# Optimization experiments

Hardware: AMD Instinct MI355X
Metric: run time of the kernel (lower is better)

The kernel has to match this reference:

```python
import jax, jax.numpy as jnp
import numpy as np

N_NODES = 100000
N_EDGES = 1000000
D = 64            # in_channels == heads*hidden_channels
OUT = 64          # out_channels
L = 3             # local_layers
RVQ = 3           # residual VQ levels per layer
CODES = 16
BN_EPS = 1e-5
COMMIT_W = 0.25


def _l2n(v, eps=1e-12):
    return v / (jnp.linalg.norm(v, axis=-1, keepdims=True) + eps)


def setup_inputs() -> dict:
    key = jax.random.key(0)
    ks = jax.random.split(key, 16)
    s = 1.0 / np.sqrt(D)
    inp = {
        "x": jax.random.normal(ks[0], (N_NODES, D), jnp.float32),
        "edge_index": jax.random.randint(ks[1], (2, N_EDGES), 0, N_NODES, jnp.int64),
        # SAGEConv: lin_l (applied to mean-aggregated neighbors, with bias), lin_r (root, no bias)
        "Wa": jax.random.uniform(ks[2], (L, D, D), jnp.float32, -s, s),
        "ba": jax.random.uniform(ks[3], (L, D), jnp.float32, -s, s),
        "Wr": jax.random.uniform(ks[4], (L, D, D), jnp.float32, -s, s),
        # skip Linear per layer
        "Wl": jax.random.uniform(ks[5], (L, D, D), jnp.float32, -s, s),
        "bl": jax.random.uniform(ks[6], (L, D), jnp.float32, -s, s),
        # BatchNorm affine
        "gamma": jnp.ones((L, D), jnp.float32),
        "beta": jnp.zeros((L, D), jnp.float32),
        # residual-VQ codebooks: [layer, rvq_level, codes, dim]
        "codebooks": jax.random.normal(ks[7], (L, RVQ, CODES, D), jnp.float32),
        # heads
        "Wp": jax.random.uniform(ks[8], (D, OUT), jnp.float32, -s, s),
        "bp": jax.random.uniform(ks[9], (OUT,), jnp.float32, -s, s),
        "Wg": jax.random.uniform(ks[10], (D, L * RVQ), jnp.float32, -s, s),
        "bg": jax.random.uniform(ks[11], (L * RVQ,), jnp.float32, -s, s),
    }
    return inp


def _sage_conv(x, src, dst, Wa, ba, Wr):
    # mean aggregation of source features onto destinations
    summed = jax.ops.segment_sum(x[src], dst, num_segments=N_NODES)
    cnt = jax.ops.segment_sum(jnp.ones((src.shape[0],), x.dtype), dst, num_segments=N_NODES)
    mean = summed / jnp.maximum(cnt, 1.0)[:, None]
    out = mean @ Wa + ba + x @ Wr
    return _l2n(out)  # normalize=True


def _residual_vq(x, cbs):
    # cosine-sim residual VQ, 3 levels; returns (quantized_sum, ids [N,RVQ], commit_loss)
    residual = x
    quant = jnp.zeros_like(x)
    loss = jnp.zeros((), x.dtype)
    ids = []
    for r in range(RVQ):
        cb = _l2n(cbs[r])                       # [CODES, D]
        sim = _l2n(residual) @ cb.T             # [N, CODES]
        idx = jnp.argmax(sim, axis=-1)          # [N]
        q = cb[idx]                             # [N, D]
        loss = loss + COMMIT_W * jnp.mean((jax.lax.stop_gradient(q) - residual) ** 2)
        q_st = residual + jax.lax.stop_gradient(q - residual)  # straight-through
        quant = quant + q_st
        residual = residual - jax.lax.stop_gradient(q)
        ids.append(idx)
    return quant, jnp.stack(ids, axis=1), loss


def reference(x, edge_index, Wa, ba, Wr, Wl, bl, gamma, beta, codebooks, Wp, bp, Wg, bg):
    src, dst = edge_index[0], edge_index[1]
    h = x  # in_dropout: identity at inference
    x_local = jnp.zeros((N_NODES, D), x.dtype)
    total_commit = jnp.zeros((), x.dtype)
    id_list = []
    for i in range(L):
        h = _sage_conv(h, src, dst, Wa[i], ba[i], Wr[i]) + (h @ Wl[i] + bl[i])
        # BatchNorm1d (batch statistics)
        mu = jnp.mean(h, axis=0)
        var = jnp.var(h, axis=0)
        h = (h - mu) * jax.lax.rsqrt(var + BN_EPS) * gamma[i] + beta[i]
        h = jax.nn.relu(h)  # dropout: identity at inference
        x_local = x_local + h
        _, ids, closs = _residual_vq(h, codebooks[i])
        total_commit = total_commit + closs
        id_list.append(ids)
    id_concat = jnp.concatenate(id_list, axis=1)  # [N, L*RVQ]
    gnn_id = x_local @ Wg + bg
    pred = x_local @ Wp + bp
    return (pred, total_commit, id_concat, gnn_id)
```

## Files before the change

kernel.cpp:

```cpp
#include <hip/hip_runtime.h>
#include <math.h>

#define NN 100000
#define NE 1000000
#define D 64
#define L 3
#define RVQ 3
#define CODES 16
#define BN_EPS 1e-5f
#define COMMIT_W 0.25f

#define GRID_A 2048

#define OFS_ROWPTR 0
#define OFS_CNT    100016
#define OFS_CURSOR 200032
#define OFS_BSUMS  300048
#define OFS_BOFFS  300176
#define OFS_STATS  300304
#define OFS_CSR    300800
#define OFS_HA     1300800
#define OFS_HB     7700800
#define OFS_XLOC   14100800
#define OFS_PART   20500800

#define OUT_PRED   0
#define OUT_COMMIT (NN * D)
#define OUT_IDS    (NN * D + 1)
#define OUT_GNN    (NN * D + 1 + NN * (L * RVQ))

static __device__ __forceinline__ float waveSum(float v) {
    #pragma unroll
    for (int off = 32; off; off >>= 1) v += __shfl_xor(v, off, 64);
    return v;
}

static __device__ __forceinline__ float qxor1(float v) {
    return __int_as_float(__builtin_amdgcn_mov_dpp(__float_as_int(v), 0xB1, 0xF, 0xF, 1));
}
static __device__ __forceinline__ float qxor2(float v) {
    return __int_as_float(__builtin_amdgcn_mov_dpp(__float_as_int(v), 0x4E, 0xF, 0xF, 1));
}

__global__ void k_count(const int* __restrict__ dst, int* __restrict__ cnt) {
    int e = blockIdx.x * blockDim.x + threadIdx.x;
    if (e < NE) atomicAdd(&cnt[dst[e]], 1);
}

#define SCAN_B 1024
__global__ void k_scan1(const int* __restrict__ cnt, int* __restrict__ rowptr,
                        int* __restrict__ bsums) {
    __shared__ int sm[SCAN_B];
    int t = threadIdx.x;
    int i = blockIdx.x * SCAN_B + t;
    int v = (i < NN) ? cnt[i] : 0;
    sm[t] = v;
    __syncthreads();
    for (int off = 1; off < SCAN_B; off <<= 1) {
        int add = (t >= off) ? sm[t - off] : 0;
        __syncthreads();
        sm[t] += add;
        __syncthreads();
    }
    if (i < NN) rowptr[i + 1] = sm[t];
    if (t == SCAN_B - 1) bsums[blockIdx.x] = sm[t];
}

__global__ void k_scan2(const int* __restrict__ bsums, int* __restrict__ boffs, int nb) {
    __shared__ int sm[SCAN_B];
    int t = threadIdx.x;
    int orig = (t < nb) ? bsums[t] : 0;
    sm[t] = orig;
    __syncthreads();
    for (int off = 1; off < SCAN_B; off <<= 1) {
        int add = (t >= off) ? sm[t - off] : 0;
        __syncthreads();
        sm[t] += add;
        __syncthreads();
    }
    if (t < nb) boffs[t] = sm[t] - orig;
}

__global__ void k_scan3(int* __restrict__ rowptr, const int* __restrict__ boffs) {
    int i = blockIdx.x * SCAN_B + threadIdx.x;
    if (i < NN) rowptr[i + 1] += boffs[blockIdx.x];
    if (i == 0) rowptr[0] = 0;
}

__global__ void k_cursor(const int* __restrict__ rowptr, int* __restrict__ cursor) {
    int i = blockIdx.x * blockDim.x + threadIdx.x;
    if (i < NN) cursor[i] = rowptr[i];
}

__global__ void k_fill(const int* __restrict__ src, const int* __restrict__ dst,
                       int* __restrict__ cursor, int* __restrict__ csr_src) {
    int e = blockIdx.x * blockDim.x + threadIdx.x;
    if (e < NE) {
        int p = atomicAdd(&cursor[dst[e]], 1);
        csr_src[p] = src[e];
    }
}

__global__ void k_sortrows(const int* __restrict__ rowptr, int* __restrict__ csr) {
    int n = blockIdx.x * blockDim.x + threadIdx.x;
    if (n >= NN) return;
    int r0 = rowptr[n], r1 = rowptr[n + 1];
    for (int i = r0 + 1; i < r1; ++i) {
        int v = csr[i];
        int j = i - 1;
        while (j >= r0 && csr[j] > v) { csr[j + 1] = csr[j]; --j; }
        csr[j + 1] = v;
    }
}

__global__ __launch_bounds__(256) void k_gather(
    const float* __restrict__ h, const int* __restrict__ rowptr,
    const int* __restrict__ csr_src, float* __restrict__ mean_out) {
    int t = threadIdx.x;
    int lane = t & 63, wid = t >> 6;
    int n = blockIdx.x * 4 + wid;
    if (n >= NN) return;

    int r0 = rowptr[n], r1 = rowptr[n + 1];
    float s = 0.f;
    for (int base = r0; base < r1; base += 64) {
        int last = r1 - 1;
        int ii = base + lane;
        int idx = csr_src[(ii <= last) ? ii : last];
        int m = r1 - base;
        if (m > 64) m = 64;
        int j = 0;
        for (; j + 8 <= m; j += 8) {
            int i0 = __shfl(idx, j + 0, 64), i1 = __shfl(idx, j + 1, 64);
            int i2 = __shfl(idx, j + 2, 64), i3 = __shfl(idx, j + 3, 64);
            int i4 = __shfl(idx, j + 4, 64), i5 = __shfl(idx, j + 5, 64);
            int i6 = __shfl(idx, j + 6, 64), i7 = __shfl(idx, j + 7, 64);
            float v0 = h[i0 * D + lane], v1 = h[i1 * D + lane];
            float v2 = h[i2 * D + lane], v3 = h[i3 * D + lane];
            float v4 = h[i4 * D + lane], v5 = h[i5 * D + lane];
            float v6 = h[i6 * D + lane], v7 = h[i7 * D + lane];
            s += v0; s += v1; s += v2; s += v3;
            s += v4; s += v5; s += v6; s += v7;
        }
        for (; j + 4 <= m; j += 4) {
            int i0 = __shfl(idx, j + 0, 64), i1 = __shfl(idx, j + 1, 64);
            int i2 = __shfl(idx, j + 2, 64), i3 = __shfl(idx, j + 3, 64);
            float v0 = h[i0 * D + lane], v1 = h[i1 * D + lane];
            float v2 = h[i2 * D + lane], v3 = h[i3 * D + lane];
            s += v0; s += v1; s += v2; s += v3;
        }
        for (; j < m; ++j) {
            int i0 = __shfl(idx, j, 64);
            s += h[i0 * D + lane];
        }
    }
    float deg = (float)(r1 - r0);
    mean_out[n * D + lane] = s / fmaxf(deg, 1.0f);
}

__global__ __launch_bounds__(256) void k_matvec(
    const float* __restrict__ mean, const float* __restrict__ h,
    float* __restrict__ hp,
    const float* __restrict__ Wa, const float* __restrict__ ba,
    const float* __restrict__ Wr, const float* __restrict__ Wl,
    const float* __restrict__ bl) {
    int t = threadIdx.x, lane = t & 63, wid = t >> 6;
    int tb = (blockIdx.x * 4 + wid) * 8;
    if (tb >= NN) return;
    int nu = __builtin_amdgcn_readfirstlane(tb);

    float bav = ba[lane], blv = bl[lane];

    float am[8], rm[8], lm[8];
    #pragma unroll
    for (int i = 0; i < 8; ++i) { am[i] = 0.f; rm[i] = 0.f; lm[i] = 0.f; }

    #pragma unroll 1
    for (int c = 0; c < 8; ++c) {
        float wa8[8], wr8[8], wl8[8];
        #pragma unroll
        for (int j = 0; j < 8; ++j) {
            wa8[j] = Wa[(c * 8 + j) * D + lane];
            wr8[j] = Wr[(c * 8 + j) * D + lane];
            wl8[j] = Wl[(c * 8 + j) * D + lane];
        }
        #pragma unroll
        for (int i = 0; i < 8; ++i) {
            const float4* mb = (const float4*)(mean + (size_t)(nu + i) * D + c * 8);
            const float4* hb = (const float4*)(h    + (size_t)(nu + i) * D + c * 8);
            float4 m0 = mb[0], m1 = mb[1];
            float4 h0 = hb[0], h1 = hb[1];
            am[i] += m0.x * wa8[0]; rm[i] += h0.x * wr8[0]; lm[i] += h0.x * wl8[0];
            am[i] += m0.y * wa8[1]; rm[i] += h0.y * wr8[1]; lm[i] += h0.y * wl8[1];
            am[i] += m0.z * wa8[2]; rm[i] += h0.z * wr8[2]; lm[i] += h0.z * wl8[2];
            am[i] += m0.w * wa8[3]; rm[i] += h0.w * wr8[3]; lm[i] += h0.w * wl8[3];
            am[i] += m1.x * wa8[4]; rm[i] += h1.x * wr8[4]; lm[i] += h1.x * wl8[4];
            am[i] += m1.y * wa8[5]; rm[i] += h1.y * wr8[5]; lm[i] += h1.y * wl8[5];
            am[i] += m1.z * wa8[6]; rm[i] += h1.z * wr8[6]; lm[i] += h1.z * wl8[6];
            am[i] += m1.w * wa8[7]; rm[i] += h1.w * wr8[7]; lm[i] += h1.w * wl8[7];
        }
    }

    #pragma unroll
    for (int i = 0; i < 8; ++i) {
        float sage = am[i] + bav + rm[i];
        float ss = waveSum(sage * sage);
        float inv = 1.0f / (sqrtf(ss) + 1e-12f);
        float hpv = sage * inv + lm[i] + blv;
        hp[(size_t)(tb + i) * D + lane] = hpv;
    }
}

__global__ __launch_bounds__(256) void k_bnstats(
    const float* __restrict__ hp, float* __restrict__ partials) {
    __shared__ float red[2][4][D];
    int t = threadIdx.x, lane = t & 63, wid = t >> 6;
    int wg = blockIdx.x * 4 + wid;
    const int wstep = GRID_A * 4;
    float accS = 0.f, accQ = 0.f;
    for (int n = wg; n < NN; n += wstep) {
        float hpv = hp[(size_t)n * D + lane];
        accS += hpv;
        accQ += hpv * hpv;
    }
    red[0][wid][lane] = accS;
    red[1][wid][lane] = accQ;
    __syncthreads();
    if (wid == 0) {
        float s0 = (red[0][0][lane] + red[0][1][lane]) + (red[0][2][lane] + red[0][3][lane]);
        float q0 = (red[1][0][lane] + red[1][1][lane]) + (red[1][2][lane] + red[1][3][lane]);
        partials[blockIdx.x * 128 + lane]      = s0;
        partials[blockIdx.x * 128 + 64 + lane] = q0;
    }
}

__global__ __launch_bounds__(256) void k_red_stats(
    const float* __restrict__ part, float* __restrict__ stats) {
    __shared__ float sm[256];
    int c = blockIdx.x;
    int i = threadIdx.x;
    float s = 0.f;
    #pragma unroll
    for (int k = 0; k < 8; ++k)
        s += part[(size_t)(i * 8 + k) * 128 + c];
    sm[i] = s;
    __syncthreads();
    #pragma unroll
    for (int off = 128; off >= 1; off >>= 1) {
        if (i < off) sm[i] += sm[i + off];
        __syncthreads();
    }
    if (i == 0) stats[c] = sm[0];
}

#define CBSTRIDE 68
__global__ __launch_bounds__(256) void k_layer_b(
    float* __restrict__ hp,
    const float* __restrict__ stats,
    const float* __restrict__ gamma, const float* __restrict__ beta,
    const float* __restrict__ cbs,
    float* __restrict__ x_local,
    float* __restrict__ ids_out,
    int layer, float* __restrict__ commit, int first_layer) {
    __shared__ alignas(16) float scb[RVQ * CODES * CBSTRIDE];
    __shared__ alignas(16) float sscale[D];
    __shared__ alignas(16) float sshift[D];
    __shared__ float sred[4];
    int t = threadIdx.x, lane = t & 63, wid = t >> 6;

    for (int row = wid; row < RVQ * CODES; row += 4) {
        float v = cbs[row * D + lane];
        float ss = waveSum(v * v);
        scb[row * CBSTRIDE + lane] = v / (sqrtf(ss) + 1e-12f);
    }
    if (t < D) {
        float mu = stats[t] * (1.0f / NN);
        float var = stats[64 + t] * (1.0f / NN) - mu * mu;
        float scale = rsqrtf(var + BN_EPS) * gamma[t];
        sscale[t] = scale;
        sshift[t] = beta[t] - mu * scale;
    }
    __syncthreads();

    int gid = blockIdx.x * 256 + t;
    int node = gid >> 2;
    int part = t & 3;
    float closs = 0.f;

    if (node < NN) {
        float res[16];
        size_t base = (size_t)node * D + part * 16;
        const float4* hr = (const float4*)(hp + base);
        float4* hw = (float4*)(hp + base);
        float4* xw = (float4*)(x_local + base);
        const float4* scp = (const float4*)(sscale + part * 16);
        const float4* shp = (const float4*)(sshift + part * 16);

        #pragma unroll
        for (int i = 0; i < 4; ++i) {
            float4 v = hr[i];
            float4 sc = scp[i], sh = shp[i];
            float4 hn;
            hn.x = fmaxf(v.x * sc.x + sh.x, 0.f);
            hn.y = fmaxf(v.y * sc.y + sh.y, 0.f);
            hn.z = fmaxf(v.z * sc.z + sh.z, 0.f);
            hn.w = fmaxf(v.w * sc.w + sh.w, 0.f);
            hw[i] = hn;
            if (first_layer) {
                xw[i] = hn;
            } else {
                float4 xl = xw[i];
                xl.x += hn.x; xl.y += hn.y; xl.z += hn.z; xl.w += hn.w;
                xw[i] = xl;
            }
            res[4 * i + 0] = hn.x; res[4 * i + 1] = hn.y;
            res[4 * i + 2] = hn.z; res[4 * i + 3] = hn.w;
        }

        int bis[RVQ];
        #pragma unroll
        for (int r = 0; r < RVQ; ++r) {
            float sims[CODES];
            #pragma unroll
            for (int j = 0; j < CODES; ++j) {
                const float* cr = &scb[(r * CODES + j) * CBSTRIDE + part * 16];
                float4 c0 = *(const float4*)(cr + 0);
                float4 c1 = *(const float4*)(cr + 4);
                float4 c2 = *(const float4*)(cr + 8);
                float4 c3 = *(const float4*)(cr + 12);
                float a = res[0] * c0.x;
                a += res[1] * c0.y;  a += res[2] * c0.z;  a += res[3] * c0.w;
                a += res[4] * c1.x;  a += res[5] * c1.y;  a += res[6] * c1.z;  a += res[7] * c1.w;
                a += res[8] * c2.x;  a += res[9] * c2.y;  a += res[10] * c2.z; a += res[11] * c2.w;
                a += res[12] * c3.x; a += res[13] * c3.y; a += res[14] * c3.z; a += res[15] * c3.w;
                float b = a + qxor1(a);
                sims[j] = b + qxor2(b);
            }
            float bv = sims[0];
            int bi = 0;
            #pragma unroll
            for (int j = 1; j < CODES; ++j)
                if (sims[j] > bv) { bv = sims[j]; bi = j; }

            const float* qr = &scb[(r * CODES + bi) * CBSTRIDE + part * 16];
            #pragma unroll
            for (int i = 0; i < 4; ++i) {
                float4 q = *(const float4*)(qr + 4 * i);
                float d0 = q.x - res[4 * i + 0]; closs += d0 * d0; res[4 * i + 0] = -d0;
                float d1 = q.y - res[4 * i + 1]; closs += d1 * d1; res[4 * i + 1] = -d1;
                float d2 = q.z - res[4 * i + 2]; closs += d2 * d2; res[4 * i + 2] = -d2;
                float d3 = q.w - res[4 * i + 3]; closs += d3 * d3; res[4 * i + 3] = -d3;
            }
            bis[r] = bi;
        }
        if (part == 0) {
            ids_out[(size_t)node * (L * RVQ) + layer * RVQ + 0] = (float)bis[0];
            ids_out[(size_t)node * (L * RVQ) + layer * RVQ + 1] = (float)bis[1];
            ids_out[(size_t)node * (L * RVQ) + layer * RVQ + 2] = (float)bis[2];
        }
    }

    closs = waveSum(closs);
    if (lane == 0) sred[wid] = closs;
    __syncthreads();
    if (t == 0) {
        float tot = (sred[0] + sred[1]) + (sred[2] + sred[3]);
        atomicAdd(commit, tot * (COMMIT_W / (float)(NN * D)));
    }
}

__global__ __launch_bounds__(256, 2) void k_head(
    const float* __restrict__ x_local,
    const float* __restrict__ Wp, const float* __restrict__ bp,
    const float* __restrict__ Wg, const float* __restrict__ bg,
    float* __restrict__ pred, float* __restrict__ gnn) {
    int t = threadIdx.x, lane = t & 63, wid = t >> 6;
    int jsafe = (lane < 9) ? lane : 0;

    float wp[D], wg[D];
    #pragma unroll
    for (int k = 0; k < D; ++k) {
        wp[k] = Wp[k * D + lane];
        wg[k] = Wg[k * 9 + jsafe];
    }
    float bpv = bp[lane], bgv = bg[jsafe];

    int w = blockIdx.x * 4 + wid;
    int wstep = gridDim.x * 4;
    for (int n = w; n < NN; n += wstep) {
        int nu = __builtin_amdgcn_readfirstlane(n);
        const float4* xrow = (const float4*)(x_local + (size_t)nu * D);
        float p = 0.f, g = 0.f;
        #pragma unroll
        for (int j = 0; j < 16; ++j) {
            float4 x4 = xrow[j];
            p += x4.x * wp[4 * j + 0]; g += x4.x * wg[4 * j + 0];
            p += x4.y * wp[4 * j + 1]; g += x4.y * wg[4 * j + 1];
            p += x4.z * wp[4 * j + 2]; g += x4.z * wg[4 * j + 2];
            p += x4.w * wp[4 * j + 3]; g += x4.w * wg[4 * j + 3];
        }
        pred[(size_t)n * D + lane] = p + bpv;
        if (lane < 9) gnn[(size_t)n * 9 + lane] = g + bgv;
    }
}

extern "C" void kernel_launch(void* const* d_in, const int* in_sizes, int n_in,
                              void* d_out, int out_size, void* d_ws, size_t ws_size,
                              hipStream_t stream) {
    const float* x   = (const float*)d_in[0];
    const int* ei    = (const int*)d_in[1];
    const float* Wa  = (const float*)d_in[2];
    const float* ba  = (const float*)d_in[3];
    const float* Wr  = (const float*)d_in[4];
    const float* Wl  = (const float*)d_in[5];
    const float* bl  = (const float*)d_in[6];
    const float* gamma = (const float*)d_in[7];
    const float* beta  = (const float*)d_in[8];
    const float* cbs = (const float*)d_in[9];
    const float* Wp  = (const float*)d_in[10];
    const float* bp  = (const float*)d_in[11];
    const float* Wg  = (const float*)d_in[12];
    const float* bg  = (const float*)d_in[13];

    const int* src = ei;
    const int* dst = ei + NE;

    int*   ws_i  = (int*)d_ws;
    float* ws_f  = (float*)d_ws;
    int* rowptr  = ws_i + OFS_ROWPTR;
    int* cnt     = ws_i + OFS_CNT;
    int* cursor  = ws_i + OFS_CURSOR;
    int* bsums   = ws_i + OFS_BSUMS;
    int* boffs   = ws_i + OFS_BOFFS;
    float* stats = ws_f + OFS_STATS;
    int* csr_src = ws_i + OFS_CSR;
    float* hA    = ws_f + OFS_HA;
    float* hB    = ws_f + OFS_HB;
    float* xloc  = ws_f + OFS_XLOC;
    float* part  = ws_f + OFS_PART;

    float* out    = (float*)d_out;
    float* pred   = out + OUT_PRED;
    float* commit = out + OUT_COMMIT;
    float* ids    = out + OUT_IDS;
    float* gnn    = out + OUT_GNN;

    float* meanb = pred;

    hipMemsetAsync(cnt, 0, NN * sizeof(int), stream);
    hipMemsetAsync(commit, 0, sizeof(float), stream);

    k_count<<<(NE + 255) / 256, 256, 0, stream>>>(dst, cnt);
    int nscan = (NN + SCAN_B - 1) / SCAN_B;
    k_scan1<<<nscan, SCAN_B, 0, stream>>>(cnt, rowptr, bsums);
    k_scan2<<<1, SCAN_B, 0, stream>>>(bsums, boffs, nscan);
    k_scan3<<<nscan, SCAN_B, 0, stream>>>(rowptr, boffs);
    k_cursor<<<(NN + 1023) / 1024, 1024, 0, stream>>>(rowptr, cursor);
    k_fill<<<(NE + 255) / 256, 256, 0, stream>>>(src, dst, cursor, csr_src);
    k_sortrows<<<(NN + 255) / 256, 256, 0, stream>>>(rowptr, csr_src);

    const float* hin = x;
    float* bufs[2] = {hA, hB};
    const int nblk_mv = NN / 32;
    const int nblk_b  = (NN * 4 + 255) / 256;
    for (int i = 0; i < L; ++i) {
        float* hout = bufs[i & 1];
        k_gather<<<(NN + 3) / 4, 256, 0, stream>>>(hin, rowptr, csr_src, meanb);
        k_matvec<<<nblk_mv, 256, 0, stream>>>(meanb, hin, hout,
                                              Wa + i * D * D, ba + i * D,
                                              Wr + i * D * D, Wl + i * D * D, bl + i * D);
        k_bnstats<<<GRID_A, 256, 0, stream>>>(hout, part);
        k_red_stats<<<128, 256, 0, stream>>>(part, stats + i * 128);
        k_layer_b<<<nblk_b, 256, 0, stream>>>(hout, stats + i * 128,
                                              gamma + i * D, beta + i * D,
                                              cbs + i * RVQ * CODES * D,
                                              xloc, ids, i, commit, (i == 0) ? 1 : 0);
        hin = hout;
    }

    k_head<<<2048, 256, 0, stream>>>(xloc, Wp, bp, Wg, bg, pred, gnn);
}
```

Measured before the change: 920.6 us.

## Restructure SAGE matvec to stage node tiles in LDS with transposed uniform weights

The matvec kernel now loads a 64-node tile of mean and h rows into shared memory. Each lane owns one node and each wave computes 8 output channels, reading transposed weights as wave-uniform scalar loads. A small per-layer kernel transposes Wa/Wr/Wl into a workspace buffer that reuses the cursor region, which is dead after CSR build. The goal is to cut the redundant per-lane global weight loads and uncoalesced row reads, at the cost of an extra launch, LDS round-trips for the output transpose, and higher register pressure with 32-element k arrays.

```diff
diff --git a/kernel.cpp b/kernel.cpp
--- a/kernel.cpp
+++ b/kernel.cpp
@@ -158,56 +158,90 @@
     mean_out[n * D + lane] = s / fmaxf(deg, 1.0f);
 }
 
-__global__ __launch_bounds__(256) void k_matvec(
+__global__ void k_wt(const float* __restrict__ Wa, const float* __restrict__ Wr,
+                     const float* __restrict__ Wl, float* __restrict__ wt) {
+    int i = blockIdx.x * 256 + threadIdx.x;
+    if (i >= 3 * D * D) return;
+    int m = i >> 12;
+    int o = (i >> 6) & 63;
+    int k = i & 63;
+    const float* W = (m == 0) ? Wa : (m == 1) ? Wr : Wl;
+    wt[i] = W[k * D + o];
+}
+
+__global__ __launch_bounds__(512) void k_matvec(
     const float* __restrict__ mean, const float* __restrict__ h,
-    float* __restrict__ hp,
-    const float* __restrict__ Wa, const float* __restrict__ ba,
-    const float* __restrict__ Wr, const float* __restrict__ Wl,
-    const float* __restrict__ bl) {
+    float* __restrict__ hp, const float* __restrict__ wt,
+    const float* __restrict__ ba, const float* __restrict__ bl) {
+    __shared__ alignas(16) float ls[64 * 132];
     int t = threadIdx.x, lane = t & 63, wid = t >> 6;
-    int tb = (blockIdx.x * 4 + wid) * 8;
-    if (tb >= NN) return;
-    int nu = __builtin_amdgcn_readfirstlane(tb);
-
-    float bav = ba[lane], blv = bl[lane];
+    int tb = blockIdx.x * 64;
+
+    #pragma unroll
+    for (int s = 0; s < 2; ++s) {
+        int fid = s * 512 + t;
+        int node = fid >> 4, c = (fid & 15) * 4;
+        int gn = tb + node; if (gn > NN - 1) gn = NN - 1;
+        float4 vm = *(const float4*)(mean + (size_t)gn * D + c);
+        float4 vh = *(const float4*)(h    + (size_t)gn * D + c);
+        *(float4*)&ls[node * 132 + c]      = vm;
+        *(float4*)&ls[node * 132 + 64 + c] = vh;
+    }
+    __syncthreads();
+
+    int ob = __builtin_amdgcn_readfirstlane(wid * 8);
 
     float am[8], rm[8], lm[8];
     #pragma unroll
-    for (int i = 0; i < 8; ++i) { am[i] = 0.f; rm[i] = 0.f; lm[i] = 0.f; }
-
-    #pragma unroll 1
-    for (int c = 0; c < 8; ++c) {
-        float wa8[8], wr8[8], wl8[8];
+    for (int oi = 0; oi < 8; ++oi) { am[oi] = 0.f; rm[oi] = 0.f; lm[oi] = 0.f; }
+
+    #pragma unroll
+    for (int half = 0; half < 2; ++half) {
+        float mk[32], hk[32];
         #pragma unroll
-        for (int j = 0; j < 8; ++j) {
-            wa8[j] = Wa[(c * 8 + j) * D + lane];
-            wr8[j] = Wr[(c * 8 + j) * D + lane];
-            wl8[j] = Wl[(c * 8 + j) * D + lane];
+        for (int q = 0; q < 8; ++q) {
+            float4 v = *(const float4*)&ls[lane * 132 + half * 32 + 4 * q];
+            mk[4 * q + 0] = v.x; mk[4 * q + 1] = v.y;
+            mk[4 * q + 2] = v.z; mk[4 * q + 3] = v.w;
+            float4 w = *(const float4*)&ls[lane * 132 + 64 + half * 32 + 4 * q];
+            hk[4 * q + 0] = w.x; hk[4 * q + 1] = w.y;
+            hk[4 * q + 2] = w.z; hk[4 * q + 3] = w.w;
         }
         #pragma unroll
-        for (int i = 0; i < 8; ++i) {
-            const float4* mb = (const float4*)(mean + (size_t)(nu + i) * D + c * 8);
-            const float4* hb = (const float4*)(h    + (size_t)(nu + i) * D + c * 8);
-            float4 m0 = mb[0], m1 = mb[1];
-            float4 h0 = hb[0], h1 = hb[1];
-            am[i] += m0.x * wa8[0]; rm[i] += h0.x * wr8[0]; lm[i] += h0.x * wl8[0];
-            am[i] += m0.y * wa8[1]; rm[i] += h0.y * wr8[1]; lm[i] += h0.y * wl8[1];
-            am[i] += m0.z * wa8[2]; rm[i] += h0.z * wr8[2]; lm[i] += h0.z * wl8[2];
-            am[i] += m0.w * wa8[3]; rm[i] += h0.w * wr8[3]; lm[i] += h0.w * wl8[3];
-            am[i] += m1.x * wa8[4]; rm[i] += h1.x * wr8[4]; lm[i] += h1.x * wl8[4];
-            am[i] += m1.y * wa8[5]; rm[i] += h1.y * wr8[5]; lm[i] += h1.y * wl8[5];
-            am[i] += m1.z * wa8[6]; rm[i] += h1.z * wr8[6]; lm[i] += h1.z * wl8[6];
-            am[i] += m1.w * wa8[7]; rm[i] += h1.w * wr8[7]; lm[i] += h1.w * wl8[7];
-        }
-    }
-
+        for (int oi = 0; oi < 8; ++oi) {
+            const float* wa = wt +        (ob + oi) * D + half * 32;
+            const float* wr = wt + 4096 + (ob + oi) * D + half * 32;
+            const float* wl = wt + 8192 + (ob + oi) * D + half * 32;
+            #pragma unroll
+            for (int k = 0; k < 32; ++k) {
+                am[oi] += mk[k] * wa[k];
+                rm[oi] += hk[k] * wr[k];
+                lm[oi] += hk[k] * wl[k];
+            }
+        }
+    }
+    __syncthreads();
+
+    #pragma unroll
+    for (int oi = 0; oi < 8; ++oi) {
+        float bav = ba[ob + oi];
+        float sage = am[oi] + bav + rm[oi];
+        ls[lane * 66 + (ob + oi)]        = sage;
+        ls[4224 + lane * 66 + (ob + oi)] = lm[oi];
+    }
+    __syncthreads();
+
+    float blv = bl[lane];
     #pragma unroll
     for (int i = 0; i < 8; ++i) {
-        float sage = am[i] + bav + rm[i];
+        int node = wid * 8 + i;
+        float sage = ls[node * 66 + lane];
+        float lv   = ls[4224 + node * 66 + lane];
         float ss = waveSum(sage * sage);
         float inv = 1.0f / (sqrtf(ss) + 1e-12f);
-        float hpv = sage * inv + lm[i] + blv;
-        hp[(size_t)(tb + i) * D + lane] = hpv;
+        float hpv = sage * inv + lv + blv;
+        int gn = tb + node;
+        if (gn < NN) hp[(size_t)gn * D + lane] = hpv;
     }
 }
 
@@ -438,6 +472,7 @@
     float* hB    = ws_f + OFS_HB;
     float* xloc  = ws_f + OFS_XLOC;
     float* part  = ws_f + OFS_PART;
+    float* wtbuf = ws_f + OFS_CURSOR;
 
     float* out    = (float*)d_out;
     float* pred   = out + OUT_PRED;
@@ -461,14 +496,15 @@
 
     const float* hin = x;
     float* bufs[2] = {hA, hB};
-    const int nblk_mv = NN / 32;
+    const int nblk_mv = (NN + 63) / 64;
     const int nblk_b  = (NN * 4 + 255) / 256;
     for (int i = 0; i < L; ++i) {
         float* hout = bufs[i & 1];
         k_gather<<<(NN + 3) / 4, 256, 0, stream>>>(hin, rowptr, csr_src, meanb);
-        k_matvec<<<nblk_mv, 256, 0, stream>>>(meanb, hin, hout,
-                                              Wa + i * D * D, ba + i * D,
-                                              Wr + i * D * D, Wl + i * D * D, bl + i * D);
+        k_wt<<<(3 * D * D + 255) / 256, 256, 0, stream>>>(Wa + i * D * D, Wr + i * D * D,
+                                                          Wl + i * D * D, wtbuf);
+        k_matvec<<<nblk_mv, 512, 0, stream>>>(meanb, hin, hout, wtbuf,
+                                              ba + i * D, bl + i * D);
         k_bnstats<<<GRID_A, 256, 0, stream>>>(hout, part);
         k_red_stats<<<128, 256, 0, stream>>>(part, stats + i * 128);
         k_layer_b<<<nblk_b, 256, 0, stream>>>(hout, stats + i * 128,
```

New measurement: 863.0 us. 6.3% less time.
